# Optimization experiments

Measured on AMD Instinct MI355X. Metric: run time of the kernel, lower is better.

The kernel has to match this reference:

```python
import jax, jax.numpy as jnp
import numpy as np

# cfg constants (match init_kwargs)
K_CFG = 32
SPOT_K = 16
K_NN = max(K_CFG + 1, SPOT_K)  # = 33
DOWN_K = 8
SIGMA_C = 3.0
SEED_NUM = 128
SEED_THRESHOLD = 0.5

B, N, M, NC, MC = 1, 4096, 4096, 512, 512
CF, CC, H = 256, 1024, 256


def pairwise_sqdist(x, y):
    # x:(B,n,3) y:(B,m,3) -> (B,n,m) squared euclidean distance
    xx = jnp.sum(x * x, -1, keepdims=True)          # (B,n,1)
    yy = jnp.sum(y * y, -1, keepdims=True)          # (B,m,1)
    return xx - 2.0 * jnp.einsum('bnd,bmd->bnm', x, y) + jnp.swapaxes(yy, 1, 2)


def knn_idx(d, k):
    # smallest-k indices along last dim
    return jax.lax.top_k(-d, k)[1]


def compatibility(ref_d, src_d, mi):
    # ref_d:(B,N,N) src_d:(B,M,M) mi:(B,N) int -> (B,N) mean compatibility
    g = jnp.take_along_axis(src_d, mi[:, :, None], axis=1)   # (B,N,M) rows gathered
    g = jnp.take_along_axis(g, mi[:, None, :], axis=2)       # (B,N,N) cols gathered
    return jnp.mean(jax.nn.relu(1.0 - jnp.abs(ref_d - g) / SIGMA_C), axis=-1)


def seeding(compat, conf):
    # faithful to torch: selection = compat < max(compat)*threshold, weighted by confidence
    # jit-friendly fixed-size topk (seed_num) instead of data-dependent max_num
    sel = (compat < compat.max(-1, keepdims=True) * SEED_THRESHOLD).astype(conf.dtype)
    return jax.lax.top_k(sel * conf, SEED_NUM)[1]            # (B,SEED_NUM)


def setup_inputs() -> dict:
    key = jax.random.key(0)
    ks = jax.random.split(key, 12)
    inp = {
        'ref_points': jax.random.normal(ks[0], (B, N, 3), jnp.float32),
        'src_points': jax.random.normal(ks[1], (B, M, 3), jnp.float32),
        'ref_feats': jax.random.normal(ks[2], (B, N, CF), jnp.float32),
        'src_feats': jax.random.normal(ks[3], (B, M, CF), jnp.float32),
        'ref_points_c': jax.random.normal(ks[4], (B, NC, 3), jnp.float32),
        'src_points_c': jax.random.normal(ks[5], (B, MC, 3), jnp.float32),
        'ref_feats_c': jax.random.normal(ks[6], (B, NC, CC), jnp.float32),
        'src_feats_c': jax.random.normal(ks[7], (B, MC, CC), jnp.float32),
        'W1': jax.random.normal(ks[8], (CC, H), jnp.float32) / np.sqrt(CC),
        'b1': jnp.zeros((H,), jnp.float32),
        'W2': jax.random.normal(ks[9], (CF, H), jnp.float32) / np.sqrt(CF),
        'b2': jnp.zeros((H,), jnp.float32),
    }
    return inp


def reference(ref_points, src_points, ref_feats, src_feats,
              ref_points_c, src_points_c, ref_feats_c, src_feats_c,
              W1, b1, W2, b2):
    # --- KNN neighbor search (torch.no_grad block) ---
    ref_dists = pairwise_sqdist(ref_points, ref_points)     # (B,N,N)
    src_dists = pairwise_sqdist(src_points, src_points)     # (B,M,M)
    ref_idx = knn_idx(ref_dists, K_NN)                      # (B,N,K_NN)
    src_idx = knn_idx(src_dists, K_NN)
    ref_idx_up = knn_idx(pairwise_sqdist(ref_points, ref_points_c), 1)[..., 0]   # (B,N)
    src_idx_up = knn_idx(pairwise_sqdist(src_points, src_points_c), 1)[..., 0]
    ref_idx_down = knn_idx(pairwise_sqdist(ref_points_c, ref_points), DOWN_K)    # (B,NC,DOWN_K)
    src_idx_down = knn_idx(pairwise_sqdist(src_points_c, src_points), DOWN_K)

    # --- input projections ---
    hf_ref = ref_feats @ W2 + b2                            # (B,N,H)
    hf_src = src_feats @ W2 + b2
    hc_ref = ref_feats_c @ W1 + b1                          # (B,NC,H)
    hc_src = src_feats_c @ W1 + b1

    # --- dual-softmax matching scores ---
    scores = jnp.einsum('bnc,bmc->bnm', hf_ref, hf_src)     # (B,N,M)
    scores = jax.nn.softmax(scores, axis=-1) * jax.nn.softmax(scores, axis=-2)

    # --- ref -> src direction ---
    conf_r = jnp.max(scores, axis=-1)                       # (B,N)
    mi_r = jnp.argmax(scores, axis=-1)                      # (B,N)
    compat_r = compatibility(ref_dists, src_dists, mi_r)    # (B,N)
    seed_r = seeding(compat_r, conf_r * compat_r)           # (B,SEED_NUM)
    spot_r = jnp.take_along_axis(src_idx[..., :SPOT_K], mi_r[:, :, None], axis=1)  # (B,N,SPOT_K)

    # --- src -> ref direction ---
    scores_t = jnp.swapaxes(scores, 1, 2)
    conf_s = jnp.max(scores_t, axis=-1)
    mi_s = jnp.argmax(scores_t, axis=-1)
    compat_s = compatibility(src_dists, ref_dists, mi_s)
    seed_s = seeding(compat_s, conf_s * compat_s)
    spot_s = jnp.take_along_axis(ref_idx[..., :SPOT_K], mi_s[:, :, None], axis=1)

    return (scores, compat_r, compat_s, seed_r, seed_s, spot_r, spot_s,
            hc_ref, hc_src, ref_idx_up, src_idx_up, ref_idx_down, src_idx_down)
```

## Files before the change

### kernel.cpp

```cpp
#include <hip/hip_runtime.h>
#include <math.h>

#define NP 4096
#define NCP 512
#define HD 256
#define CCD 1024
#define SPOTK 16
#define DOWNK 8
#define SEEDN 128
#define JCH 512
#define NJC (NP / JCH)

__global__ __launch_bounds__(256) void gemm128_bt(
    const float* __restrict__ A, const float* __restrict__ B,
    float* __restrict__ C, int M, int N, int K)
{
    const int PAD = 132;
    __shared__ float As[16 * 132];
    __shared__ float Bs[16 * 132];

    const int bm = blockIdx.y * 128, bn = blockIdx.x * 128;
    const int t = threadIdx.x;
    const int tx = t & 15, ty = t >> 4;

    float acc[2][2][4][4] = {};

    for (int k0 = 0; k0 < K; k0 += 16) {
#pragma unroll
        for (int it = 0; it < 2; it++) {
            int idx = t + it * 256;
            int row = idx >> 2, kc = (idx & 3) * 4;
            float4 v = *(const float4*)&A[(size_t)(bm + row) * K + k0 + kc];
            As[(kc + 0) * PAD + row] = v.x;
            As[(kc + 1) * PAD + row] = v.y;
            As[(kc + 2) * PAD + row] = v.z;
            As[(kc + 3) * PAD + row] = v.w;
        }
#pragma unroll
        for (int it = 0; it < 2; it++) {
            int idx = t + it * 256;
            int row = idx >> 2, kc = (idx & 3) * 4;
            float4 v = *(const float4*)&B[(size_t)(bn + row) * K + k0 + kc];
            Bs[(kc + 0) * PAD + row] = v.x;
            Bs[(kc + 1) * PAD + row] = v.y;
            Bs[(kc + 2) * PAD + row] = v.z;
            Bs[(kc + 3) * PAD + row] = v.w;
        }
        __syncthreads();
#pragma unroll
        for (int kk = 0; kk < 16; kk++) {
            float4 a0 = *(const float4*)&As[kk * PAD + ty * 4];
            float4 a1 = *(const float4*)&As[kk * PAD + ty * 4 + 64];
            float4 b0 = *(const float4*)&Bs[kk * PAD + tx * 4];
            float4 b1 = *(const float4*)&Bs[kk * PAD + tx * 4 + 64];
            float ar[2][4] = {{a0.x, a0.y, a0.z, a0.w}, {a1.x, a1.y, a1.z, a1.w}};
            float br[2][4] = {{b0.x, b0.y, b0.z, b0.w}, {b1.x, b1.y, b1.z, b1.w}};
#pragma unroll
            for (int qr = 0; qr < 2; qr++)
#pragma unroll
                for (int qc = 0; qc < 2; qc++)
#pragma unroll
                    for (int i = 0; i < 4; i++)
#pragma unroll
                        for (int j = 0; j < 4; j++)
                            acc[qr][qc][i][j] = fmaf(ar[qr][i], br[qc][j], acc[qr][qc][i][j]);
        }
        __syncthreads();
    }
#pragma unroll
    for (int qr = 0; qr < 2; qr++)
#pragma unroll
        for (int i = 0; i < 4; i++) {
            int m = bm + qr * 64 + ty * 4 + i;
#pragma unroll
            for (int qc = 0; qc < 2; qc++) {
                int n = bn + qc * 64 + tx * 4;
                float4 v = make_float4(acc[qr][qc][i][0], acc[qr][qc][i][1],
                                       acc[qr][qc][i][2], acc[qr][qc][i][3]);
                *(float4*)&C[(size_t)m * N + n] = v;
            }
        }
}

__global__ __launch_bounds__(256) void gemm64(
    const float* __restrict__ A0, const float* __restrict__ A1,
    const float* __restrict__ B, const float* __restrict__ bias,
    float* __restrict__ C0, float* __restrict__ C1,
    int M, int N, int K)
{
    const float* A = blockIdx.z ? A1 : A0;
    float* C = blockIdx.z ? C1 : C0;

    const int PAD = 68;
    __shared__ float As[16 * 68];
    __shared__ float Bs[16 * 68];

    const int bm = blockIdx.y * 64, bn = blockIdx.x * 64;
    const int t = threadIdx.x;
    const int tx = t & 15, ty = t >> 4;

    float acc[4][4] = {};

    for (int k0 = 0; k0 < K; k0 += 16) {
        {
            int row = t >> 2, kc = (t & 3) * 4;
            float4 v = *(const float4*)&A[(size_t)(bm + row) * K + k0 + kc];
            As[(kc + 0) * PAD + row] = v.x;
            As[(kc + 1) * PAD + row] = v.y;
            As[(kc + 2) * PAD + row] = v.z;
            As[(kc + 3) * PAD + row] = v.w;
        }
        {
            int k = t >> 4, n4 = (t & 15) * 4;
            float4 v = *(const float4*)&B[(size_t)(k0 + k) * N + bn + n4];
            *(float4*)&Bs[k * PAD + n4] = v;
        }
        __syncthreads();
#pragma unroll
        for (int kk = 0; kk < 16; kk++) {
            float4 a4 = *(const float4*)&As[kk * PAD + ty * 4];
            float4 b4 = *(const float4*)&Bs[kk * PAD + tx * 4];
            float ar[4] = {a4.x, a4.y, a4.z, a4.w};
            float br[4] = {b4.x, b4.y, b4.z, b4.w};
#pragma unroll
            for (int i = 0; i < 4; i++)
#pragma unroll
                for (int j = 0; j < 4; j++)
                    acc[i][j] = fmaf(ar[i], br[j], acc[i][j]);
        }
        __syncthreads();
    }
    float4 b4 = *(const float4*)&bias[bn + tx * 4];
#pragma unroll
    for (int i = 0; i < 4; i++) {
        int m = bm + ty * 4 + i;
        float4 v = make_float4(acc[i][0] + b4.x, acc[i][1] + b4.y,
                               acc[i][2] + b4.z, acc[i][3] + b4.w);
        *(float4*)&C[(size_t)m * N + bn + tx * 4] = v;
    }
}

__global__ __launch_bounds__(256) void gemm64_atomic(
    const float* __restrict__ A0, const float* __restrict__ A1,
    const float* __restrict__ B,
    float* __restrict__ C0, float* __restrict__ C1,
    int M, int N, int K, int KCH)
{
    int pair = blockIdx.z >> 3, ks = blockIdx.z & 7;
    const float* A = pair ? A1 : A0;
    float* C = pair ? C1 : C0;

    const int PAD = 68;
    __shared__ float As[16 * 68];
    __shared__ float Bs[16 * 68];

    const int bm = blockIdx.y * 64, bn = blockIdx.x * 64;
    const int t = threadIdx.x;
    const int tx = t & 15, ty = t >> 4;
    const int kbeg = ks * KCH, kend = kbeg + KCH;

    float acc[4][4] = {};

    for (int k0 = kbeg; k0 < kend; k0 += 16) {
        {
            int row = t >> 2, kc = (t & 3) * 4;
            float4 v = *(const float4*)&A[(size_t)(bm + row) * K + k0 + kc];
            As[(kc + 0) * PAD + row] = v.x;
            As[(kc + 1) * PAD + row] = v.y;
            As[(kc + 2) * PAD + row] = v.z;
            As[(kc + 3) * PAD + row] = v.w;
        }
        {
            int k = t >> 4, n4 = (t & 15) * 4;
            float4 v = *(const float4*)&B[(size_t)(k0 + k) * N + bn + n4];
            *(float4*)&Bs[k * PAD + n4] = v;
        }
        __syncthreads();
#pragma unroll
        for (int kk = 0; kk < 16; kk++) {
            float4 a4 = *(const float4*)&As[kk * PAD + ty * 4];
            float4 b4 = *(const float4*)&Bs[kk * PAD + tx * 4];
            float ar[4] = {a4.x, a4.y, a4.z, a4.w};
            float br[4] = {b4.x, b4.y, b4.z, b4.w};
#pragma unroll
            for (int i = 0; i < 4; i++)
#pragma unroll
                for (int j = 0; j < 4; j++)
                    acc[i][j] = fmaf(ar[i], br[j], acc[i][j]);
        }
        __syncthreads();
    }
#pragma unroll
    for (int i = 0; i < 4; i++) {
        int m = bm + ty * 4 + i;
#pragma unroll
        for (int j = 0; j < 4; j++)
            atomicAdd(&C[(size_t)m * N + bn + tx * 4 + j], acc[i][j]);
    }
}

__global__ void init_hc(const float* __restrict__ b1,
                        float* __restrict__ o_hcr, float* __restrict__ o_hcs)
{
    int idx = blockIdx.x * 256 + threadIdx.x;
    float b = b1[idx & (HD - 1)];
    o_hcr[idx] = b; o_hcs[idx] = b;
}

__global__ void pack_pts(const float* __restrict__ p0, const float* __restrict__ p1,
                         const float* __restrict__ p2, const float* __restrict__ p3,
                         float4* o0, float4* o1, float4* o2, float4* o3)
{
    int z = blockIdx.z;
    const float* p = (z == 0) ? p0 : (z == 1) ? p1 : (z == 2) ? p2 : p3;
    float4* o      = (z == 0) ? o0 : (z == 1) ? o1 : (z == 2) ? o2 : o3;
    int n = (z < 2) ? NP : NCP;
    int i = blockIdx.x * 256 + threadIdx.x;
    if (i >= n) return;
    float x = p[i * 3], y = p[i * 3 + 1], zz = p[i * 3 + 2];
    o[i] = make_float4(x, y, zz, x * x + y * y + zz * zz);
}

__global__ __launch_bounds__(256) void row_stats(const float* __restrict__ s,
                                                 float* rmax, float* rsum)
{
    int n = blockIdx.x;
    const float* row = s + (size_t)n * NP;
    __shared__ float red[256];
    float m = -INFINITY;
    for (int j = threadIdx.x; j < NP; j += 256) m = fmaxf(m, row[j]);
    red[threadIdx.x] = m; __syncthreads();
    for (int off = 128; off; off >>= 1) {
        if (threadIdx.x < off) red[threadIdx.x] = fmaxf(red[threadIdx.x], red[threadIdx.x + off]);
        __syncthreads();
    }
    m = red[0]; __syncthreads();
    float sum = 0.f;
    for (int j = threadIdx.x; j < NP; j += 256) sum += expf(row[j] - m);
    red[threadIdx.x] = sum; __syncthreads();
    for (int off = 128; off; off >>= 1) {
        if (threadIdx.x < off) red[threadIdx.x] += red[threadIdx.x + off];
        __syncthreads();
    }
    if (threadIdx.x == 0) { rmax[n] = m; rsum[n] = red[0]; }
}

__global__ __launch_bounds__(256) void col_stats_partial(const float* __restrict__ s,
                                                         float* pmax, float* psum)
{
    int m = blockIdx.x * 256 + threadIdx.x;
    int n0 = blockIdx.y * 128;
    float mx = -INFINITY;
    for (int n = n0; n < n0 + 128; n++) mx = fmaxf(mx, s[(size_t)n * NP + m]);
    float sum = 0.f;
    for (int n = n0; n < n0 + 128; n++) sum += expf(s[(size_t)n * NP + m] - mx);
    pmax[(size_t)blockIdx.y * NP + m] = mx;
    psum[(size_t)blockIdx.y * NP + m] = sum;
}

__global__ __launch_bounds__(256) void col_stats_combine(const float* __restrict__ pmax,
                                                         const float* __restrict__ psum,
                                                         float* cmax, float* csum)
{
    int m = blockIdx.x * 256 + threadIdx.x;
    float mx = -INFINITY;
    for (int c = 0; c < 32; c++) mx = fmaxf(mx, pmax[(size_t)c * NP + m]);
    float sum = 0.f;
    for (int c = 0; c < 32; c++) sum += psum[(size_t)c * NP + m] * expf(pmax[(size_t)c * NP + m] - mx);
    cmax[m] = mx; csum[m] = sum;
}

__global__ __launch_bounds__(256) void finalize_rows(float* __restrict__ s,
    const float* __restrict__ rmax, const float* __restrict__ rsum,
    const float* __restrict__ cmax, const float* __restrict__ csum,
    float* __restrict__ confr, int* __restrict__ mir)
{
    int n = blockIdx.x;
    float rm = rmax[n], rs = rsum[n];
    size_t base = (size_t)n * NP;
    float best = -INFINITY; int bi = 0x7fffffff;
    for (int m1 = threadIdx.x; m1 < NP; m1 += 256) {
        float v = s[base + m1];
        float a = expf(v - rm) / rs;
        float b = expf(v - cmax[m1]) / csum[m1];
        float sc = a * b;
        s[base + m1] = sc;
        if (sc > best) { best = sc; bi = m1; }
    }
    __shared__ float rv[256]; __shared__ int ri[256];
    rv[threadIdx.x] = best; ri[threadIdx.x] = bi; __syncthreads();
    for (int off = 128; off; off >>= 1) {
        if (threadIdx.x < off) {
            float v2 = rv[threadIdx.x + off]; int i2 = ri[threadIdx.x + off];
            if (v2 > rv[threadIdx.x] || (v2 == rv[threadIdx.x] && i2 < ri[threadIdx.x])) {
                rv[threadIdx.x] = v2; ri[threadIdx.x] = i2;
            }
        }
        __syncthreads();
    }
    if (threadIdx.x == 0) { confr[n] = rv[0]; mir[n] = ri[0]; }
}

__global__ __launch_bounds__(256) void col_argmax_partial(const float* __restrict__ s,
                                                          float* pconf, int* pmi)
{
    int m = blockIdx.x * 256 + threadIdx.x;
    int n0 = blockIdx.y * 128;
    float best = -INFINITY; int bi = 0;
    for (int n = n0; n < n0 + 128; n++) {
        float v = s[(size_t)n * NP + m];
        if (v > best) { best = v; bi = n; }
    }
    pconf[(size_t)blockIdx.y * NP + m] = best;
    pmi[(size_t)blockIdx.y * NP + m] = bi;
}

__global__ __launch_bounds__(256) void col_argmax_combine(const float* __restrict__ pconf,
                                                          const int* __restrict__ pmi,
                                                          float* confs, int* mis)
{
    int m = blockIdx.x * 256 + threadIdx.x;
    float best = -INFINITY; int bi = 0;
    for (int c = 0; c < 32; c++) {
        float v = pconf[(size_t)c * NP + m];
        if (v > best) { best = v; bi = pmi[(size_t)c * NP + m]; }
    }
    confs[m] = best; mis[m] = bi;
}

__global__ void gather_pts(const float4* __restrict__ p4A, const float4* __restrict__ p4B,
                           const int* __restrict__ miA, const int* __restrict__ miB,
                           float4* __restrict__ qA, float4* __restrict__ qB)
{
    const float4* p4 = blockIdx.z ? p4B : p4A;
    const int*    mi = blockIdx.z ? miB : miA;
    float4*       q  = blockIdx.z ? qB : qA;
    int j = blockIdx.x * 256 + threadIdx.x;
    if (j >= NP) return;
    q[j] = p4[mi[j]];
}

__global__ __launch_bounds__(256) void compat_kernel(
    const float4* __restrict__ baseA, const float4* __restrict__ baseB,
    const float4* __restrict__ qA, const float4* __restrict__ qB,
    float* __restrict__ o1A, float* __restrict__ o1B,
    float* __restrict__ o2A, float* __restrict__ o2B)
{
    const float4* base = blockIdx.z ? baseB : baseA;
    const float4* q    = blockIdx.z ? qB : qA;
    float* out1        = blockIdx.z ? o1B : o1A;
    float* out2        = blockIdx.z ? o2B : o2A;
    int n = blockIdx.x;
    float4 b = base[n];
    float4 a = q[n];
    float sum = 0.f;
    for (int j = threadIdx.x; j < NP; j += 256) {
        float4 p = base[j];
        float rt = b.x * p.x + b.y * p.y + b.z * p.z;
        float rd = (b.w - 2.f * rt) + p.w;
        float4 qj = q[j];
        float st = a.x * qj.x + a.y * qj.y + a.z * qj.z;
        float sd = (a.w - 2.f * st) + qj.w;
        float c = 1.f - fabsf(rd - sd) / 3.0f;
        sum += fmaxf(c, 0.f);
    }
    __shared__ float red[256];
    red[threadIdx.x] = sum; __syncthreads();
    for (int off = 128; off; off >>= 1) {
        if (threadIdx.x < off) red[threadIdx.x] += red[threadIdx.x + off];
        __syncthreads();
    }
    if (threadIdx.x == 0) { float c = red[0] * (1.0f / NP); out1[n] = c; out2[n] = c; }
}

__global__ __launch_bounds__(256) void seed_prep(
    const float* __restrict__ compatA, const float* __restrict__ compatB,
    const float* __restrict__ confA, const float* __restrict__ confB,
    float* __restrict__ wA, float* __restrict__ wB)
{
    const float* compat = blockIdx.z ? compatB : compatA;
    const float* conf   = blockIdx.z ? confB : confA;
    float* w            = blockIdx.z ? wB : wA;
    __shared__ float red[256];
    int tid = threadIdx.x;
    float mx = -INFINITY;
    for (int j = tid; j < NP; j += 256) mx = fmaxf(mx, compat[j]);
    red[tid] = mx; __syncthreads();
    for (int off = 128; off; off >>= 1) {
        if (tid < off) red[tid] = fmaxf(red[tid], red[tid + off]);
        __syncthreads();
    }
    float thr = red[0] * 0.5f;
    for (int j = tid; j < NP; j += 256) {
        float c = compat[j];
        w[j] = (c < thr) ? conf[j] * c : 0.0f;
    }
}

__global__ __launch_bounds__(256) void seed_rank_partial(
    const float* __restrict__ wA, const float* __restrict__ wB,
    int* __restrict__ rankpA, int* __restrict__ rankpB)
{
    const float* w = blockIdx.z ? wB : wA;
    int* rankp     = blockIdx.z ? rankpB : rankpA;
    int tid = threadIdx.x;
    int jc = blockIdx.y;

    __shared__ float4 wj[JCH / 4];
    if (tid < JCH / 4) wj[tid] = ((const float4*)w)[jc * (JCH / 4) + tid];
    __syncthreads();

    int i = blockIdx.x * 256 + tid;
    float wi = w[i];
    int jbase = jc * JCH;
    int r0 = 0, r1 = 0, r2 = 0, r3 = 0;
#pragma unroll 4
    for (int j4 = 0; j4 < JCH / 4; j4++) {
        float4 v = wj[j4];
        int j = jbase + j4 * 4;
        r0 += (v.x > wi || (v.x == wi && (j    ) < i));
        r1 += (v.y > wi || (v.y == wi && (j + 1) < i));
        r2 += (v.z > wi || (v.z == wi && (j + 2) < i));
        r3 += (v.w > wi || (v.w == wi && (j + 3) < i));
    }
    rankp[(size_t)jc * NP + i] = (r0 + r1) + (r2 + r3);
}

__global__ __launch_bounds__(256) void seed_scatter(
    const int* __restrict__ rankpA, const int* __restrict__ rankpB,
    float* __restrict__ outA, float* __restrict__ outB)
{
    const int* rankp = blockIdx.z ? rankpB : rankpA;
    float* outp      = blockIdx.z ? outB : outA;
    int i = blockIdx.x * 256 + threadIdx.x;
    int r = 0;
#pragma unroll
    for (int jc = 0; jc < NJC; jc++) r += rankp[(size_t)jc * NP + i];
    if (r < SEEDN) outp[r] = (float)i;
}

__device__ __forceinline__ void bitonic64_val(float& d, int lane)
{
#pragma unroll
    for (int k = 2; k <= 64; k <<= 1)
#pragma unroll
        for (int j = k >> 1; j > 0; j >>= 1) {
            float od = __shfl_xor(d, j);
            bool lower = ((lane & j) == 0);
            bool asc   = ((lane & k) == 0);
            bool take = (lower == asc) ? (od < d) : (d < od);
            d = take ? od : d;
        }
}

__device__ __forceinline__ void bitonic64_lex(float& d, int& i, int lane)
{
#pragma unroll
    for (int k = 2; k <= 64; k <<= 1)
#pragma unroll
        for (int j = k >> 1; j > 0; j >>= 1) {
            float od = __shfl_xor(d, j);
            int   oi = __shfl_xor(i, j);
            bool lower = ((lane & j) == 0);
            bool asc   = ((lane & k) == 0);
            bool less = (od < d) || (od == d && oi < i);
            bool gtr  = (d < od) || (d == od && i < oi);
            bool take = (lower == asc) ? less : gtr;
            d = take ? od : d;
            i = take ? oi : i;
        }
}

template<int KSEL>
__device__ __forceinline__ void merge_chunk(float& run_d, int& run_i,
                                            float cd, int ci, int lane)
{
    bitonic64_lex(cd, ci, lane);
    int src = lane - KSEL;
    int s2 = (src >= 0 && src < KSEL) ? src : 0;
    float cd2 = __shfl(cd, s2);
    int   ci2 = __shfl(ci, s2);
    float nd = (lane < KSEL) ? run_d : ((lane < 2 * KSEL) ? cd2 : INFINITY);
    int   ni = (lane < KSEL) ? run_i : ((lane < 2 * KSEL) ? ci2 : 0x7fffffff);
    bitonic64_lex(nd, ni, lane);
    run_d = nd; run_i = ni;
}

template<int KSEL>
__global__ __launch_bounds__(256) void knn_topk(
    const float4* __restrict__ rowA, const float4* __restrict__ rowB,
    const float4* __restrict__ colA, const float4* __restrict__ colB,
    int ncols,
    int* __restrict__ outiA, int* __restrict__ outiB,
    float* __restrict__ outfA, float* __restrict__ outfB)
{
    const float4* rowp = blockIdx.z ? rowB : rowA;
    const float4* colp = blockIdx.z ? colB : colA;
    int* outi = blockIdx.z ? outiB : outiA;
    float* outf = blockIdx.z ? outfB : outfA;

    int wid = threadIdx.x >> 6, lane = threadIdx.x & 63;
    int r = blockIdx.x * 4 + wid;

    float4 p = rowp[r];

    float mn = INFINITY;
    for (int j0 = 0; j0 < ncols; j0 += 64) {
        float4 c = colp[j0 + lane];
        float t = p.x * c.x + p.y * c.y + p.z * c.z;
        float d = (p.w - 2.f * t) + c.w;
        mn = fminf(mn, d);
    }
    bitonic64_val(mn, lane);
    float T = __shfl(mn, KSEL - 1) + 1e-4f;

    __shared__ float qd[4][256];
    __shared__ int   qi[4][256];
    int cnt = 0; bool ovf = false;
    for (int j0 = 0; j0 < ncols; j0 += 64) {
        int j = j0 + lane;
        float4 c = colp[j];
        float t = p.x * c.x + p.y * c.y + p.z * c.z;
        float d = (p.w - 2.f * t) + c.w;
        bool keep = (d <= T);
        unsigned long long mask = __ballot(keep);
        int nsel = __popcll(mask);
        if (cnt + nsel > 256) { ovf = true; break; }
        if (keep) {
            int pos = cnt + (int)__popcll(mask & ((1ull << lane) - 1ull));
            qd[wid][pos] = d; qi[wid][pos] = j;
        }
        cnt += nsel;
    }

    float run_d = INFINITY; int run_i = 0x7fffffff;
    if (!ovf) {
        for (int c = 0; c < cnt; c += 64) {
            int idx = c + lane;
            float cd = (idx < cnt) ? qd[wid][idx] : INFINITY;
            int   ci = (idx < cnt) ? qi[wid][idx] : 0x7fffffff;
            merge_chunk<KSEL>(run_d, run_i, cd, ci, lane);
        }
    } else {
        for (int j0 = 0; j0 < ncols; j0 += 64) {
            int j = j0 + lane;
            float4 c = colp[j];
            float t = p.x * c.x + p.y * c.y + p.z * c.z;
            float d = (p.w - 2.f * t) + c.w;
            merge_chunk<KSEL>(run_d, run_i, d, j, lane);
        }
    }

    if (lane < KSEL) {
        if (outi) outi[(size_t)r * KSEL + lane] = run_i;
        else      outf[(size_t)r * KSEL + lane] = (float)run_i;
    }
}

__global__ __launch_bounds__(256) void up_argmin(
    const float4* __restrict__ ptsA, const float4* __restrict__ ptsB,
    const float4* __restrict__ ptscA, const float4* __restrict__ ptscB,
    float* __restrict__ outA, float* __restrict__ outB)
{
    const float4* pts   = blockIdx.z ? ptsB : ptsA;
    const float4* pts_c = blockIdx.z ? ptscB : ptscA;
    float* out_f        = blockIdx.z ? outB : outA;
    __shared__ float4 cp[NCP];
    for (int c = threadIdx.x; c < NCP; c += 256) cp[c] = pts_c[c];
    __syncthreads();
    int n = blockIdx.x * 256 + threadIdx.x;
    float4 p = pts[n];
    float best = INFINITY; int bi = 0;
    for (int c = 0; c < NCP; c++) {
        float4 q = cp[c];
        float t = p.x * q.x + p.y * q.y + p.z * q.z;
        float d = (p.w - 2.f * t) + q.w;
        if (d < best) { best = d; bi = c; }
    }
    out_f[n] = (float)bi;
}

__global__ void spot_gather(const int* __restrict__ idxA, const int* __restrict__ idxB,
                            const int* __restrict__ miA, const int* __restrict__ miB,
                            float* __restrict__ outA, float* __restrict__ outB)
{
    const int* idx16 = blockIdx.z ? idxB : idxA;
    const int* mi    = blockIdx.z ? miB : miA;
    float* outp      = blockIdx.z ? outB : outA;
    int t = blockIdx.x * 256 + threadIdx.x;
    int n = t >> 4, k = t & 15;
    outp[t] = (float)idx16[(size_t)mi[n] * SPOTK + k];
}

extern "C" void kernel_launch(void* const* d_in, const int* in_sizes, int n_in,
                              void* d_out, int out_size, void* d_ws, size_t ws_size,
                              hipStream_t stream)
{
    const float* ref_points   = (const float*)d_in[0];
    const float* src_points   = (const float*)d_in[1];
    const float* ref_feats    = (const float*)d_in[2];
    const float* src_feats    = (const float*)d_in[3];
    const float* ref_points_c = (const float*)d_in[4];
    const float* src_points_c = (const float*)d_in[5];
    const float* ref_feats_c  = (const float*)d_in[6];
    const float* src_feats_c  = (const float*)d_in[7];
    const float* W1 = (const float*)d_in[8];
    const float* b1 = (const float*)d_in[9];
    const float* W2 = (const float*)d_in[10];
    const float* b2 = (const float*)d_in[11];

    float* out = (float*)d_out;
    float* o_scores = out;
    float* o_compr  = o_scores + (size_t)NP * NP;
    float* o_comps  = o_compr + NP;
    float* o_seedr  = o_comps + NP;
    float* o_seeds  = o_seedr + SEEDN;
    float* o_spotr  = o_seeds + SEEDN;
    float* o_spots  = o_spotr + (size_t)NP * SPOTK;
    float* o_hcr    = o_spots + (size_t)NP * SPOTK;
    float* o_hcs    = o_hcr + (size_t)NCP * HD;
    float* o_rup    = o_hcs + (size_t)NCP * HD;
    float* o_sup    = o_rup + NP;
    float* o_rdown  = o_sup + NP;
    float* o_sdown  = o_rdown + (size_t)NCP * DOWNK;

    float* ws = (float*)d_ws;
    float* hfr   = ws;
    float* hfs   = hfr + (size_t)NP * HD;
    float* rmax  = hfs + (size_t)NP * HD;
    float* rsum  = rmax + NP;
    float* cmax  = rsum + NP;
    float* csum  = cmax + NP;
    float* confr = csum + NP;
    float* confs = confr + NP;
    float* compr = confs + NP;
    float* comps = compr + NP;
    int*   mir   = (int*)(comps + NP);
    int*   mis   = mir + NP;
    float* pmax  = (float*)(mis + NP);
    float* psum  = pmax + 32 * NP;
    float* pconf = psum + 32 * NP;
    int*   pmi   = (int*)(pconf + 32 * NP);
    float4* qr   = (float4*)(pmi + 32 * NP);
    float4* qs   = qr + NP;
    int* ridx16  = (int*)(qs + NP);
    int* sidx16  = ridx16 + (size_t)NP * SPOTK;
    float4* rp4  = (float4*)(sidx16 + (size_t)NP * SPOTK);
    float4* sp4  = rp4 + NP;
    float4* rcp4 = sp4 + NP;
    float4* scp4 = rcp4 + NCP;
    float* wA    = (float*)(scp4 + NCP);
    float* wB    = wA + NP;
    int* rankpA  = (int*)(wB + NP);
    int* rankpB  = rankpA + NJC * NP;
    size_t ws_need = (size_t)((float*)(rankpB + NJC * NP) - ws) * 4;
    if (ws_size < ws_need) return;

    dim3 b256(256);

    pack_pts<<<dim3(NP / 256, 1, 4), b256, 0, stream>>>(
        ref_points, src_points, ref_points_c, src_points_c, rp4, sp4, rcp4, scp4);

    init_hc<<<dim3((NCP * HD) / 256), b256, 0, stream>>>(b1, o_hcr, o_hcs);
    gemm64_atomic<<<dim3(HD / 64, NCP / 64, 16), b256, 0, stream>>>(
        ref_feats_c, src_feats_c, W1, o_hcr, o_hcs, NCP, HD, CCD, CCD / 8);

    gemm64<<<dim3(HD / 64, NP / 64, 2), b256, 0, stream>>>(
        ref_feats, src_feats, W2, b2, hfr, hfs, NP, HD, HD);

    gemm128_bt<<<dim3(32, 32, 1), b256, 0, stream>>>(
        hfr, hfs, o_scores, NP, NP, HD);

    knn_topk<SPOTK><<<dim3(NP / 4, 1, 2), b256, 0, stream>>>(
        rp4, sp4, rp4, sp4, NP, ridx16, sidx16, nullptr, nullptr);
    knn_topk<DOWNK><<<dim3(NCP / 4, 1, 2), b256, 0, stream>>>(
        rcp4, scp4, rp4, sp4, NP, nullptr, nullptr, o_rdown, o_sdown);
    up_argmin<<<dim3(NP / 256, 1, 2), b256, 0, stream>>>(
        rp4, sp4, rcp4, scp4, o_rup, o_sup);

    row_stats<<<NP, b256, 0, stream>>>(o_scores, rmax, rsum);
    col_stats_partial<<<dim3(16, 32), b256, 0, stream>>>(o_scores, pmax, psum);
    col_stats_combine<<<16, b256, 0, stream>>>(pmax, psum, cmax, csum);
    finalize_rows<<<NP, b256, 0, stream>>>(o_scores, rmax, rsum, cmax, csum, confr, mir);
    col_argmax_partial<<<dim3(16, 32), b256, 0, stream>>>(o_scores, pconf, pmi);
    col_argmax_combine<<<16, b256, 0, stream>>>(pconf, pmi, confs, mis);

    gather_pts<<<dim3(NP / 256, 1, 2), b256, 0, stream>>>(
        sp4, rp4, mir, mis, qr, qs);
    compat_kernel<<<dim3(NP, 1, 2), b256, 0, stream>>>(
        rp4, sp4, qr, qs, o_compr, o_comps, compr, comps);

    seed_prep<<<dim3(1, 1, 2), b256, 0, stream>>>(
        compr, comps, confr, confs, wA, wB);
    seed_rank_partial<<<dim3(NP / 256, NJC, 2), b256, 0, stream>>>(
        wA, wB, rankpA, rankpB);
    seed_scatter<<<dim3(NP / 256, 1, 2), b256, 0, stream>>>(
        rankpA, rankpB, o_seedr, o_seeds);

    spot_gather<<<dim3((NP * SPOTK) / 256, 1, 2), b256, 0, stream>>>(
        sidx16, ridx16, mir, mis, o_spotr, o_spots);
}
```

Measured before the change: 570.1 us.

## Fuse softmax row/column statistics into scores GEMM epilogue with register prefetch

Computes per-tile row and column max/sum-exp partials directly from GEMM accumulators using wave shuffles and shared memory. Small combine kernels then merge them, and the separate row_stats and column stats passes over the full scores matrix are removed. The GEMM also prefetches the next K-slice into registers before computing on the current one. This removes two full reads of the large score matrix, at the cost of extra epilogue work and register pressure.

Measured after the change: 521.5 us. 1.09x faster.

```diff
diff --git a/kernel.cpp b/kernel.cpp
--- a/kernel.cpp
+++ b/kernel.cpp
@@ -13,7 +13,10 @@
 
 __global__ __launch_bounds__(256) void gemm128_bt(
     const float* __restrict__ A, const float* __restrict__ B,
-    float* __restrict__ C, int M, int N, int K)
+    float* __restrict__ C,
+    float* __restrict__ pmaxR, float* __restrict__ psumR,
+    float* __restrict__ pmaxC, float* __restrict__ psumC,
+    int M, int N, int K)
 {
     const int PAD = 132;
     __shared__ float As[16 * 132];
@@ -25,28 +28,41 @@
 
     float acc[2][2][4][4] = {};
 
+    const int rowA0 = t >> 2, kcA0 = (t & 3) * 4;
+    const int rowA1 = (t + 256) >> 2, kcA1 = ((t + 256) & 3) * 4;
+
+    float4 pa0 = *(const float4*)&A[(size_t)(bm + rowA0) * K + kcA0];
+    float4 pa1 = *(const float4*)&A[(size_t)(bm + rowA1) * K + kcA1];
+    float4 pb0 = *(const float4*)&B[(size_t)(bn + rowA0) * K + kcA0];
+    float4 pb1 = *(const float4*)&B[(size_t)(bn + rowA1) * K + kcA1];
+
     for (int k0 = 0; k0 < K; k0 += 16) {
-#pragma unroll
-        for (int it = 0; it < 2; it++) {
-            int idx = t + it * 256;
-            int row = idx >> 2, kc = (idx & 3) * 4;
-            float4 v = *(const float4*)&A[(size_t)(bm + row) * K + k0 + kc];
-            As[(kc + 0) * PAD + row] = v.x;
-            As[(kc + 1) * PAD + row] = v.y;
-            As[(kc + 2) * PAD + row] = v.z;
-            As[(kc + 3) * PAD + row] = v.w;
-        }
-#pragma unroll
-        for (int it = 0; it < 2; it++) {
-            int idx = t + it * 256;
-            int row = idx >> 2, kc = (idx & 3) * 4;
-            float4 v = *(const float4*)&B[(size_t)(bn + row) * K + k0 + kc];
-            Bs[(kc + 0) * PAD + row] = v.x;
-            Bs[(kc + 1) * PAD + row] = v.y;
-            Bs[(kc + 2) * PAD + row] = v.z;
-            Bs[(kc + 3) * PAD + row] = v.w;
-        }
-        __syncthreads();
+        As[(kcA0 + 0) * PAD + rowA0] = pa0.x;
+        As[(kcA0 + 1) * PAD + rowA0] = pa0.y;
+        As[(kcA0 + 2) * PAD + rowA0] = pa0.z;
+        As[(kcA0 + 3) * PAD + rowA0] = pa0.w;
+        As[(kcA1 + 0) * PAD + rowA1] = pa1.x;
+        As[(kcA1 + 1) * PAD + rowA1] = pa1.y;
+        As[(kcA1 + 2) * PAD + rowA1] = pa1.z;
+        As[(kcA1 + 3) * PAD + rowA1] = pa1.w;
+        Bs[(kcA0 + 0) * PAD + rowA0] = pb0.x;
+        Bs[(kcA0 + 1) * PAD + rowA0] = pb0.y;
+        Bs[(kcA0 + 2) * PAD + rowA0] = pb0.z;
+        Bs[(kcA0 + 3) * PAD + rowA0] = pb0.w;
+        Bs[(kcA1 + 0) * PAD + rowA1] = pb1.x;
+        Bs[(kcA1 + 1) * PAD + rowA1] = pb1.y;
+        Bs[(kcA1 + 2) * PAD + rowA1] = pb1.z;
+        Bs[(kcA1 + 3) * PAD + rowA1] = pb1.w;
+        __syncthreads();
+
+        if (k0 + 16 < K) {
+            int kn = k0 + 16;
+            pa0 = *(const float4*)&A[(size_t)(bm + rowA0) * K + kn + kcA0];
+            pa1 = *(const float4*)&A[(size_t)(bm + rowA1) * K + kn + kcA1];
+            pb0 = *(const float4*)&B[(size_t)(bn + rowA0) * K + kn + kcA0];
+            pb1 = *(const float4*)&B[(size_t)(bn + rowA1) * K + kn + kcA1];
+        }
+
 #pragma unroll
         for (int kk = 0; kk < 16; kk++) {
             float4 a0 = *(const float4*)&As[kk * PAD + ty * 4];
@@ -67,6 +83,7 @@
         }
         __syncthreads();
     }
+
 #pragma unroll
     for (int qr = 0; qr < 2; qr++)
 #pragma unroll
@@ -80,6 +97,90 @@
                 *(float4*)&C[(size_t)m * N + n] = v;
             }
         }
+
+#pragma unroll
+    for (int qr = 0; qr < 2; qr++)
+#pragma unroll
+        for (int i = 0; i < 4; i++) {
+            float m = -INFINITY;
+#pragma unroll
+            for (int qc = 0; qc < 2; qc++)
+#pragma unroll
+                for (int j = 0; j < 4; j++) m = fmaxf(m, acc[qr][qc][i][j]);
+            float s = 0.f;
+#pragma unroll
+            for (int qc = 0; qc < 2; qc++)
+#pragma unroll
+                for (int j = 0; j < 4; j++) s += expf(acc[qr][qc][i][j] - m);
+#pragma unroll
+            for (int off = 1; off < 16; off <<= 1) {
+                float om = __shfl_xor(m, off), os = __shfl_xor(s, off);
+                float Mx = fmaxf(m, om);
+                s = s * expf(m - Mx) + os * expf(om - Mx);
+                m = Mx;
+            }
+            if (tx == 0) {
+                int r = bm + qr * 64 + ty * 4 + i;
+                pmaxR[(size_t)blockIdx.x * NP + r] = m;
+                psumR[(size_t)blockIdx.x * NP + r] = s;
+            }
+        }
+
+    float* colm = As;
+    float* cols_ = Bs;
+#pragma unroll
+    for (int qc = 0; qc < 2; qc++)
+#pragma unroll
+        for (int j = 0; j < 4; j++) {
+            float m = -INFINITY;
+#pragma unroll
+            for (int qr = 0; qr < 2; qr++)
+#pragma unroll
+                for (int i = 0; i < 4; i++) m = fmaxf(m, acc[qr][qc][i][j]);
+            float s = 0.f;
+#pragma unroll
+            for (int qr = 0; qr < 2; qr++)
+#pragma unroll
+                for (int i = 0; i < 4; i++) s += expf(acc[qr][qc][i][j] - m);
+#pragma unroll
+            for (int off = 16; off < 64; off <<= 1) {
+                float om = __shfl_xor(m, off), os = __shfl_xor(s, off);
+                float Mx = fmaxf(m, om);
+                s = s * expf(m - Mx) + os * expf(om - Mx);
+                m = Mx;
+            }
+            if ((ty & 3) == 0) {
+                int w = ty >> 2, c = qc * 64 + tx * 4 + j;
+                colm[w * 132 + c] = m;
+                cols_[w * 132 + c] = s;
+            }
+        }
+    __syncthreads();
+    if (t < 128) {
+        int c = t;
+        float m = colm[c], s = cols_[c];
+#pragma unroll
+        for (int w = 1; w < 4; w++) {
+            float om = colm[w * 132 + c], os = cols_[w * 132 + c];
+            float Mx = fmaxf(m, om);
+            s = s * expf(m - Mx) + os * expf(om - Mx);
+            m = Mx;
+        }
+        pmaxC[(size_t)blockIdx.y * NP + bn + c] = m;
+        psumC[(size_t)blockIdx.y * NP + bn + c] = s;
+    }
+}
+
+__global__ __launch_bounds__(256) void combine_stats(const float* __restrict__ pmax,
+                                                     const float* __restrict__ psum,
+                                                     float* omax, float* osum)
+{
+    int m = blockIdx.x * 256 + threadIdx.x;
+    float mx = -INFINITY;
+    for (int c = 0; c < 32; c++) mx = fmaxf(mx, pmax[(size_t)c * NP + m]);
+    float sum = 0.f;
+    for (int c = 0; c < 32; c++) sum += psum[(size_t)c * NP + m] * expf(pmax[(size_t)c * NP + m] - mx);
+    omax[m] = mx; osum[m] = sum;
 }
 
 __global__ __launch_bounds__(256) void gemm64(
@@ -219,55 +320,6 @@
     if (i >= n) return;
     float x = p[i * 3], y = p[i * 3 + 1], zz = p[i * 3 + 2];
     o[i] = make_float4(x, y, zz, x * x + y * y + zz * zz);
-}
-
-__global__ __launch_bounds__(256) void row_stats(const float* __restrict__ s,
-                                                 float* rmax, float* rsum)
-{
-    int n = blockIdx.x;
-    const float* row = s + (size_t)n * NP;
-    __shared__ float red[256];
-    float m = -INFINITY;
-    for (int j = threadIdx.x; j < NP; j += 256) m = fmaxf(m, row[j]);
-    red[threadIdx.x] = m; __syncthreads();
-    for (int off = 128; off; off >>= 1) {
-        if (threadIdx.x < off) red[threadIdx.x] = fmaxf(red[threadIdx.x], red[threadIdx.x + off]);
-        __syncthreads();
-    }
-    m = red[0]; __syncthreads();
-    float sum = 0.f;
-    for (int j = threadIdx.x; j < NP; j += 256) sum += expf(row[j] - m);
-    red[threadIdx.x] = sum; __syncthreads();
-    for (int off = 128; off; off >>= 1) {
-        if (threadIdx.x < off) red[threadIdx.x] += red[threadIdx.x + off];
-        __syncthreads();
-    }
-    if (threadIdx.x == 0) { rmax[n] = m; rsum[n] = red[0]; }
-}
-
-__global__ __launch_bounds__(256) void col_stats_partial(const float* __restrict__ s,
-                                                         float* pmax, float* psum)
-{
-    int m = blockIdx.x * 256 + threadIdx.x;
-    int n0 = blockIdx.y * 128;
-    float mx = -INFINITY;
-    for (int n = n0; n < n0 + 128; n++) mx = fmaxf(mx, s[(size_t)n * NP + m]);
-    float sum = 0.f;
-    for (int n = n0; n < n0 + 128; n++) sum += expf(s[(size_t)n * NP + m] - mx);
-    pmax[(size_t)blockIdx.y * NP + m] = mx;
-    psum[(size_t)blockIdx.y * NP + m] = sum;
-}
-
-__global__ __launch_bounds__(256) void col_stats_combine(const float* __restrict__ pmax,
-                                                         const float* __restrict__ psum,
-                                                         float* cmax, float* csum)
-{
-    int m = blockIdx.x * 256 + threadIdx.x;
-    float mx = -INFINITY;
-    for (int c = 0; c < 32; c++) mx = fmaxf(mx, pmax[(size_t)c * NP + m]);
-    float sum = 0.f;
-    for (int c = 0; c < 32; c++) sum += psum[(size_t)c * NP + m] * expf(pmax[(size_t)c * NP + m] - mx);
-    cmax[m] = mx; csum[m] = sum;
 }
 
 __global__ __launch_bounds__(256) void finalize_rows(float* __restrict__ s,
@@ -656,6 +708,9 @@
     size_t ws_need = (size_t)((float*)(rankpB + NJC * NP) - ws) * 4;
     if (ws_size < ws_need) return;
 
+    float* pmaxR = pconf;
+    float* psumR = (float*)pmi;
+
     dim3 b256(256);
 
     pack_pts<<<dim3(NP / 256, 1, 4), b256, 0, stream>>>(
@@ -669,7 +724,9 @@
         ref_feats, src_feats, W2, b2, hfr, hfs, NP, HD, HD);
 
     gemm128_bt<<<dim3(32, 32, 1), b256, 0, stream>>>(
-        hfr, hfs, o_scores, NP, NP, HD);
+        hfr, hfs, o_scores, pmaxR, psumR, pmax, psum, NP, NP, HD);
+    combine_stats<<<16, b256, 0, stream>>>(pmaxR, psumR, rmax, rsum);
+    combine_stats<<<16, b256, 0, stream>>>(pmax, psum, cmax, csum);
 
     knn_topk<SPOTK><<<dim3(NP / 4, 1, 2), b256, 0, stream>>>(
         rp4, sp4, rp4, sp4, NP, ridx16, sidx16, nullptr, nullptr);
@@ -678,9 +735,6 @@
     up_argmin<<<dim3(NP / 256, 1, 2), b256, 0, stream>>>(
         rp4, sp4, rcp4, scp4, o_rup, o_sup);
 
-    row_stats<<<NP, b256, 0, stream>>>(o_scores, rmax, rsum);
-    col_stats_partial<<<dim3(16, 32), b256, 0, stream>>>(o_scores, pmax, psum);
-    col_stats_combine<<<16, b256, 0, stream>>>(pmax, psum, cmax, csum);
     finalize_rows<<<NP, b256, 0, stream>>>(o_scores, rmax, rsum, cmax, csum, confr, mir);
     col_argmax_partial<<<dim3(16, 32), b256, 0, stream>>>(o_scores, pconf, pmi);
     col_argmax_combine<<<16, b256, 0, stream>>>(pconf, pmi, confs, mis);
```
